# Kernel tuning notes

Measured on AMD Instinct MI355X. Metric: run time of the kernel, lower is better.

Reference implementation:

```python
import jax, jax.numpy as jnp
import numpy as np

WIN = 64
SHIFT = 32
HEADS = 12


def setup_inputs() -> dict:
    key = jax.random.key(0)
    ks = jax.random.split(key, 6)
    D = 768
    return {
        'x': jax.random.normal(ks[0], (16, 4096, D), dtype=jnp.float32),
        'qkv_w': jax.random.normal(ks[1], (3 * D, D), dtype=jnp.float32) * (D ** -0.5),
        'qkv_b': jax.random.normal(ks[2], (3 * D,), dtype=jnp.float32) * 0.02,
        'proj_w': jax.random.normal(ks[3], (D, D), dtype=jnp.float32) * (D ** -0.5),
        'proj_b': jax.random.normal(ks[4], (D,), dtype=jnp.float32) * 0.02,
        'rel_bias': jax.random.normal(ks[5], (HEADS, 2 * WIN - 1), dtype=jnp.float32) * 0.02,
    }


def reference(x, qkv_w, qkv_b, proj_w, proj_b, rel_bias):
    B, N, D = x.shape
    H, hd = HEADS, D // HEADS
    scale = hd ** -0.5
    if SHIFT:
        x = jnp.roll(x, SHIFT, axis=1)
    pad = (-N) % WIN
    if pad:
        x = jnp.pad(x, ((0, 0), (0, pad), (0, 0)))
    Np = x.shape[1]
    nW = Np // WIN
    # [B*nW, w, D] windows
    xw = x.reshape(B * nW, WIN, D)
    qkv = xw @ qkv_w.T + qkv_b                       # [B*nW, w, 3D]
    qkv = qkv.reshape(B * nW, WIN, 3, H, hd).transpose(2, 0, 3, 1, 4)
    q, k, v = qkv[0], qkv[1], qkv[2]                 # [B*nW, H, w, hd]
    attn = jnp.einsum('bhqd,bhkd->bhqk', q, k) * scale
    idx = jnp.arange(WIN)
    rel = idx[None, :] - idx[:, None] + (WIN - 1)    # [w, w] in [0, 2w-2]
    attn = attn + rel_bias[:, rel][None]             # gather bias per head
    attn = jax.nn.softmax(attn, axis=-1)
    y = jnp.einsum('bhqk,bhkd->bhqd', attn, v)       # [B*nW, H, w, hd]
    y = y.transpose(0, 2, 1, 3).reshape(B * nW, WIN, D)
    y = y @ proj_w.T + proj_b
    y = y.reshape(B, Np, D)
    if pad:
        y = y[:, :N, :]
    if SHIFT:
        y = jnp.roll(y, -SHIFT, axis=1)
    return y
```

## Files before the change

### kernel.cpp

```cpp
#include <hip/hip_runtime.h>
#include <hip/hip_bf16.h>
#include <stdint.h>

#define SEQ     4096
#define NBATCH  16
#define DMODEL  768
#define NHEAD   12
#define HDIM    64
#define WINSZ   64
#define SHIFT_T 32
#define QKV_N   (3*DMODEL)

typedef __attribute__((ext_vector_type(8)))  short bf16x8;
typedef __attribute__((ext_vector_type(4)))  float f32x4;

static __device__ __forceinline__ unsigned short f2bf(float f) {
  union { float f; unsigned u; } v; v.f = f;
  unsigned r = v.u + 0x7fffu + ((v.u >> 16) & 1u);
  return (unsigned short)(r >> 16);
}

#define G2L(gp, lp) __builtin_amdgcn_global_load_lds( \
    (const __attribute__((address_space(1))) unsigned*)(const void*)(gp), \
    (__attribute__((address_space(3))) unsigned*)(void*)(lp), 16, 0, 0)

#define MFMA16(a,b,c) __builtin_amdgcn_mfma_f32_16x16x32_bf16(a,b,c,0,0,0)
#define LDS8(p) (*(const bf16x8*)(p))
#define BARR __builtin_amdgcn_s_barrier()
#define SBAR __builtin_amdgcn_sched_barrier(0)
#define LGK0 do { asm volatile("s_waitcnt lgkmcnt(0)" ::: "memory"); SBAR; } while(0)

__global__ void k_cvt_x(const float* __restrict__ x, unsigned short* __restrict__ xb,
                        long long n8) {
  for (long long i = (long long)blockIdx.x*blockDim.x + threadIdx.x; i < n8;
       i += (long long)gridDim.x*blockDim.x) {
    long long e = i*8;
    int d = (int)(e % DMODEL);
    long long gt = e / DMODEL;
    int t = (int)(gt & (SEQ-1));
    long long b = gt >> 12;
    int ts = (t - SHIFT_T) & (SEQ-1);
    const float* src = x + (((b << 12) + ts) * (long long)DMODEL + d);
    float4 a0 = *(const float4*)src;
    float4 a1 = *(const float4*)(src + 4);
    bf16x8 o;
    o[0]=(short)f2bf(a0.x); o[1]=(short)f2bf(a0.y); o[2]=(short)f2bf(a0.z); o[3]=(short)f2bf(a0.w);
    o[4]=(short)f2bf(a1.x); o[5]=(short)f2bf(a1.y); o[6]=(short)f2bf(a1.z); o[7]=(short)f2bf(a1.w);
    *(bf16x8*)(xb + e) = o;
  }
}

__global__ void k_cvt_w(const float* __restrict__ w, unsigned short* __restrict__ wb, int n8) {
  int i = blockIdx.x*blockDim.x + threadIdx.x;
  if (i >= n8) return;
  float4 a0 = ((const float4*)w)[2*i];
  float4 a1 = ((const float4*)w)[2*i+1];
  bf16x8 o;
  o[0]=(short)f2bf(a0.x); o[1]=(short)f2bf(a0.y); o[2]=(short)f2bf(a0.z); o[3]=(short)f2bf(a0.w);
  o[4]=(short)f2bf(a1.x); o[5]=(short)f2bf(a1.y); o[6]=(short)f2bf(a1.z); o[7]=(short)f2bf(a1.w);
  ((bf16x8*)wb)[i] = o;
}

template<int MODE>
__global__ __launch_bounds__(512, 1)
void k_gemm256(const unsigned short* __restrict__ A, const unsigned short* __restrict__ Bw,
               const float* __restrict__ bias, unsigned short* __restrict__ Cb,
               float* __restrict__ Cf, int M, int N, int K, int nTN, long long c0) {
  __shared__ char lds[131072];
  const int nt = K >> 6;
  int nwg = gridDim.x;
  int cpx = nwg >> 3;
  int wg  = (blockIdx.x & 7) * cpx + (blockIdx.x >> 3);
  int bm = wg / nTN, bn = wg - bm*nTN;
  long long m0 = (long long)bm * 256;
  int n0 = bn * 256;
  int tid = threadIdx.x;
  int lane = tid & 63, wid = tid >> 6;
  int wr = wid >> 2, wc = wid & 3;
  int cl = lane & 15, g4 = lane >> 4;

  const long long K2 = 2LL * K;
  int L  = tid * 16;
  int Ls = L ^ (((L >> 7) & 7) << 4);
  int srow = Ls >> 7, scol = Ls & 127;
  const char* gAr0 = (const char*)A + (m0 +       srow) * K2 + scol;
  const char* gAr1 = (const char*)A + (m0 +  64 + srow) * K2 + scol;
  const char* gAr2 = (const char*)A + (m0 + 128 + srow) * K2 + scol;
  const char* gAr3 = (const char*)A + (m0 + 192 + srow) * K2 + scol;
  const char* gBr0 = (const char*)Bw + (long long)(n0 +       srow) * K2 + scol;
  const char* gBr1 = (const char*)Bw + (long long)(n0 +  64 + srow) * K2 + scol;
  const char* gBr2 = (const char*)Bw + (long long)(n0 + 128 + srow) * K2 + scol;
  const char* gBr3 = (const char*)Bw + (long long)(n0 + 192 + srow) * K2 + scol;

  int p0 = cl*128 + ((g4*16) ^ ((cl & 7) << 4));
  int p1 = p0 ^ 64;
  int RA0 = wr*16384;
  int RA1 = wr*16384 + 8192;
  int BB  = 32768 + wc*8192;

  f32x4 acc[8][4];
  #pragma unroll
  for (int i = 0; i < 8; ++i)
    #pragma unroll
    for (int j = 0; j < 4; ++j) acc[i][j] = (f32x4){0.f,0.f,0.f,0.f};

#define MMPH(MA, MB, x0, x1, y0, y1) \
  acc[MA][0]=MFMA16(x0,b00,acc[MA][0]); acc[MA][1]=MFMA16(x0,b10,acc[MA][1]); \
  acc[MA][2]=MFMA16(x0,b20,acc[MA][2]); acc[MA][3]=MFMA16(x0,b30,acc[MA][3]); \
  acc[MB][0]=MFMA16(y0,b00,acc[MB][0]); acc[MB][1]=MFMA16(y0,b10,acc[MB][1]); \
  acc[MB][2]=MFMA16(y0,b20,acc[MB][2]); acc[MB][3]=MFMA16(y0,b30,acc[MB][3]); \
  acc[MA][0]=MFMA16(x1,b01,acc[MA][0]); acc[MA][1]=MFMA16(x1,b11,acc[MA][1]); \
  acc[MA][2]=MFMA16(x1,b21,acc[MA][2]); acc[MA][3]=MFMA16(x1,b31,acc[MA][3]); \
  acc[MB][0]=MFMA16(y1,b01,acc[MB][0]); acc[MB][1]=MFMA16(y1,b11,acc[MB][1]); \
  acc[MB][2]=MFMA16(y1,b21,acc[MB][2]); acc[MB][3]=MFMA16(y1,b31,acc[MB][3]);

#define TILE(RD, ST, DOSTAGE, WBSTR, DOWA) do {                               \
    const char* rbuf = (RD); char* stb = (ST);                                \
    bf16x8 b00,b01,b10,b11,b20,b21,b30,b31;                                   \
    { bf16x8 x0 = LDS8(rbuf + RA0        + p0), x1 = LDS8(rbuf + RA0        + p1);\
      bf16x8 y0 = LDS8(rbuf + RA0 + 2048 + p0), y1 = LDS8(rbuf + RA0 + 2048 + p1);\
      b00 = LDS8(rbuf + BB        + p0);  b01 = LDS8(rbuf + BB        + p1);  \
      b10 = LDS8(rbuf + BB + 2048 + p0);  b11 = LDS8(rbuf + BB + 2048 + p1);  \
      b20 = LDS8(rbuf + BB + 4096 + p0);  b21 = LDS8(rbuf + BB + 4096 + p1);  \
      b30 = LDS8(rbuf + BB + 6144 + p0);  b31 = LDS8(rbuf + BB + 6144 + p1);  \
      if (DOSTAGE) { G2L(gBr0, stb + 32768 + L); G2L(gBr1, stb + 40960 + L); }\
      asm volatile("s_waitcnt lgkmcnt(8)" ::: "memory"); SBAR;                \
      BARR; LGK0;                                                             \
      __builtin_amdgcn_s_setprio(1);                                          \
      MMPH(0, 1, x0, x1, y0, y1)                                              \
      __builtin_amdgcn_s_setprio(0); SBAR; BARR;                              \
    }                                                                         \
    { bf16x8 x0 = LDS8(rbuf + RA0 + 4096 + p0), x1 = LDS8(rbuf + RA0 + 4096 + p1);\
      bf16x8 y0 = LDS8(rbuf + RA0 + 6144 + p0), y1 = LDS8(rbuf + RA0 + 6144 + p1);\
      if (DOSTAGE) { G2L(gBr2, stb + 49152 + L); G2L(gBr3, stb + 57344 + L); }\
      SBAR; BARR; LGK0;                                                       \
      __builtin_amdgcn_s_setprio(1);                                          \
      MMPH(2, 3, x0, x1, y0, y1)                                              \
      __builtin_amdgcn_s_setprio(0); SBAR;                                    \
      asm volatile(WBSTR ::: "memory"); SBAR; BARR;                           \
    }                                                                         \
    { bf16x8 x0 = LDS8(rbuf + RA1        + p0), x1 = LDS8(rbuf + RA1        + p1);\
      bf16x8 y0 = LDS8(rbuf + RA1 + 2048 + p0), y1 = LDS8(rbuf + RA1 + 2048 + p1);\
      if (DOSTAGE) { G2L(gAr0, stb + L); G2L(gAr2, stb + 16384 + L); }        \
      SBAR; BARR; LGK0;                                                       \
      __builtin_amdgcn_s_setprio(1);                                          \
      MMPH(4, 5, x0, x1, y0, y1)                                              \
      __builtin_amdgcn_s_setprio(0); SBAR; BARR;                              \
    }                                                                         \
    { bf16x8 x0 = LDS8(rbuf + RA1 + 4096 + p0), x1 = LDS8(rbuf + RA1 + 4096 + p1);\
      bf16x8 y0 = LDS8(rbuf + RA1 + 6144 + p0), y1 = LDS8(rbuf + RA1 + 6144 + p1);\
      if (DOSTAGE) { G2L(gAr1, stb + 8192 + L); G2L(gAr3, stb + 24576 + L);   \
                     gAr0 += 128; gAr1 += 128; gAr2 += 128; gAr3 += 128;      \
                     gBr0 += 128; gBr1 += 128; gBr2 += 128; gBr3 += 128; }    \
      SBAR; BARR; LGK0;                                                       \
      __builtin_amdgcn_s_setprio(1);                                          \
      MMPH(6, 7, x0, x1, y0, y1)                                              \
      __builtin_amdgcn_s_setprio(0); SBAR;                                    \
      if (DOWA) { asm volatile("s_waitcnt vmcnt(2)" ::: "memory"); }          \
      SBAR; BARR;                                                             \
    }                                                                         \
  } while (0)

  G2L(gBr0, lds + 32768 + L); G2L(gBr1, lds + 40960 + L);
  G2L(gBr2, lds + 49152 + L); G2L(gBr3, lds + 57344 + L);
  G2L(gAr0, lds + L);         G2L(gAr2, lds + 16384 + L);
  G2L(gAr1, lds + 8192 + L);  G2L(gAr3, lds + 24576 + L);
  gAr0 += 128; gAr1 += 128; gAr2 += 128; gAr3 += 128;
  gBr0 += 128; gBr1 += 128; gBr2 += 128; gBr3 += 128;
  asm volatile("s_waitcnt vmcnt(2)" ::: "memory");
  SBAR; BARR;

  char* const bufA = lds;
  char* const bufB = lds + 65536;
  for (int i = 0; i < (nt - 2) / 2; ++i) {
    TILE(bufA, bufB, 1, "s_waitcnt vmcnt(4)", 1);
    TILE(bufB, bufA, 1, "s_waitcnt vmcnt(4)", 1);
  }
  TILE(bufA, bufB, 1, "s_waitcnt vmcnt(4)", 1);
  TILE(bufB, bufA, 0, "s_waitcnt vmcnt(0)", 0);
#undef TILE
#undef MMPH

  #pragma unroll
  for (int mf = 0; mf < 8; ++mf) {
    #pragma unroll
    for (int nf = 0; nf < 4; ++nf) {
      int n = n0 + wc*64 + nf*16 + cl;
      float bv = bias[n];
      #pragma unroll
      for (int r = 0; r < 4; ++r) {
        long long m = m0 + wr*128 + mf*16 + g4*4 + r;
        float v = acc[mf][nf][r] + bv;
        if (MODE == 0) {
          int nb = n0 + wc*64;
          int t  = nb / DMODEL;
          int h  = (nb - t*DMODEL) >> 6;
          long long panel = ((((m >> 6)*NHEAD + h)*3 + t) << 12);
          Cb[panel + ((m & 63) << 6) + nf*16 + cl] = f2bf(v);
        } else {
          long long gm = c0 + m;
          long long om = (gm & ~(long long)(SEQ-1)) | ((gm - SHIFT_T) & (long long)(SEQ-1));
          Cf[om * (long long)N + n] = v;
        }
      }
    }
  }
}

__global__ __launch_bounds__(256, 4)
void k_attn(const unsigned short* __restrict__ qkv, const float* __restrict__ rel_bias,
            unsigned short* __restrict__ y) {
  int w = blockIdx.x / NHEAD;
  int h = blockIdx.x - w*NHEAD;
  __shared__ unsigned short sQ[64*72], sK[64*72], sV[64*72];
  __shared__ unsigned short sP[4][16*72];
  __shared__ float rb[128];
  int tid = threadIdx.x, lane = tid & 63, wid = tid >> 6;
  int cl = lane & 15, g4 = lane >> 4;

  if (tid < 2*WINSZ - 1) rb[tid] = rel_bias[h*(2*WINSZ-1) + tid];

  const unsigned short* panel = qkv + ((long long)((w*NHEAD + h)*3) << 12);
  {
    int row = tid >> 2, c16 = (tid & 3) * 16;
    const unsigned short* s0 = panel + tid*16;
    *(bf16x8*)(sQ + row*72 + c16)     = *(const bf16x8*)(s0);
    *(bf16x8*)(sQ + row*72 + c16 + 8) = *(const bf16x8*)(s0 + 8);
    *(bf16x8*)(sK + row*72 + c16)     = *(const bf16x8*)(s0 + 4096);
    *(bf16x8*)(sK + row*72 + c16 + 8) = *(const bf16x8*)(s0 + 4096 + 8);
    *(bf16x8*)(sV + row*72 + c16)     = *(const bf16x8*)(s0 + 8192);
    *(bf16x8*)(sV + row*72 + c16 + 8) = *(const bf16x8*)(s0 + 8192 + 8);
  }
  __syncthreads();

  f32x4 sc[4];
  #pragma unroll
  for (int nt = 0; nt < 4; ++nt) sc[nt] = (f32x4){0.f,0.f,0.f,0.f};
  #pragma unroll
  for (int kk = 0; kk < 2; ++kk) {
    bf16x8 aq = *(const bf16x8*)(sQ + (wid*16 + cl)*72 + kk*32 + g4*8);
    #pragma unroll
    for (int nt = 0; nt < 4; ++nt) {
      bf16x8 bk = *(const bf16x8*)(sK + (nt*16 + cl)*72 + kk*32 + g4*8);
      sc[nt] = MFMA16(aq, bk, sc[nt]);
    }
  }

  float pv[4][4];
  #pragma unroll
  for (int r = 0; r < 4; ++r) {
    int qi = wid*16 + g4*4 + r;
    float mx = -1e30f;
    #pragma unroll
    for (int nt = 0; nt < 4; ++nt) {
      int kj = nt*16 + cl;
      float v = sc[nt][r]*0.125f + rb[kj - qi + (WINSZ-1)];
      pv[nt][r] = v;
      mx = fmaxf(mx, v);
    }
    #pragma unroll
    for (int m = 1; m < 16; m <<= 1) mx = fmaxf(mx, __shfl_xor(mx, m, 64));
    float sum = 0.f;
    #pragma unroll
    for (int nt = 0; nt < 4; ++nt) { float e = __expf(pv[nt][r]-mx); pv[nt][r] = e; sum += e; }
    #pragma unroll
    for (int m = 1; m < 16; m <<= 1) sum += __shfl_xor(sum, m, 64);
    float inv = 1.f / sum;
    #pragma unroll
    for (int nt = 0; nt < 4; ++nt)
      sP[wid][(g4*4+r)*72 + nt*16 + cl] = f2bf(pv[nt][r]*inv);
  }

  f32x4 o[4];
  #pragma unroll
  for (int nt = 0; nt < 4; ++nt) o[nt] = (f32x4){0.f,0.f,0.f,0.f};
  #pragma unroll
  for (int kk = 0; kk < 2; ++kk) {
    bf16x8 ap = *(const bf16x8*)(&sP[wid][cl*72 + kk*32 + g4*8]);
    #pragma unroll
    for (int nt = 0; nt < 4; ++nt) {
      bf16x8 bv;
      #pragma unroll
      for (int j = 0; j < 8; ++j)
        bv[j] = (short)sV[(kk*32 + g4*8 + j)*72 + nt*16 + cl];
      o[nt] = MFMA16(ap, bv, o[nt]);
    }
  }

  long long tokbase = (long long)w * WINSZ;
  #pragma unroll
  for (int nt = 0; nt < 4; ++nt)
    #pragma unroll
    for (int r = 0; r < 4; ++r) {
      int row = wid*16 + g4*4 + r;
      y[(tokbase + row) * (long long)DMODEL + h*HDIM + nt*16 + cl] = f2bf(o[nt][r]);
    }
}

extern "C" void kernel_launch(void* const* d_in, const int* in_sizes, int n_in,
                              void* d_out, int out_size, void* d_ws, size_t ws_size,
                              hipStream_t stream) {
  const float* x      = (const float*)d_in[0];
  const float* qkv_w  = (const float*)d_in[1];
  const float* qkv_b  = (const float*)d_in[2];
  const float* proj_w = (const float*)d_in[3];
  const float* proj_b = (const float*)d_in[4];
  const float* rel_b  = (const float*)d_in[5];
  float* out = (float*)d_out;

  const long long NTOK = (long long)NBATCH * SEQ;

  char* ws = (char*)d_ws;
  unsigned short* qkvb = (unsigned short*)ws;
  unsigned short* yb   = (unsigned short*)(ws + (size_t)NTOK*QKV_N*2);
  unsigned short* wq   = (unsigned short*)(ws + (size_t)NTOK*QKV_N*2 + (size_t)NTOK*DMODEL*2);
  unsigned short* wp   = wq + (size_t)QKV_N*DMODEL;

  k_cvt_w<<<(QKV_N*DMODEL/8 + 255)/256, 256, 0, stream>>>(qkv_w, wq, QKV_N*DMODEL/8);
  k_cvt_w<<<(DMODEL*DMODEL/8 + 255)/256, 256, 0, stream>>>(proj_w, wp, DMODEL*DMODEL/8);

  long long n8 = NTOK * DMODEL / 8;
  k_cvt_x<<<2048, 256, 0, stream>>>(x, yb , n8);

  int mT = (int)(NTOK / 256);
  k_gemm256<0><<<mT * (QKV_N/256), 512, 0, stream>>>(yb, wq, qkv_b, qkvb, nullptr,
                                                     (int)NTOK, QKV_N, DMODEL, QKV_N/256, 0);
  k_attn<<<(int)(NTOK/WINSZ) * NHEAD, 256, 0, stream>>>(qkvb, rel_b, yb );
  k_gemm256<1><<<mT * (DMODEL/256), 512, 0, stream>>>(yb, wp, proj_b, nullptr, out,
                                                      (int)NTOK, DMODEL, DMODEL, DMODEL/256, 0);
}
```

Measured before the change: 498.6 us.

## Add dedicated 128x256 QKV GEMM kernel with triple-buffered LDS and higher occupancy

Replaces the 256x256 tile QKV projection GEMM with a new kernel using 128x256 tiles, a 3-stage LDS ring of 24KB per stage, and launch bounds allowing several workgroups per CU. The new kernel writes bf16 output directly in the per-window head-panel layout the attention kernel reads. The generic MODE 0 epilogue now writes row-major, but that path is no longer launched. The goal is better occupancy and latency hiding for the QKV GEMM. The cost is smaller tiles with less data reuse per workgroup and more workgroups.

```diff
diff --git a/kernel.cpp b/kernel.cpp
--- a/kernel.cpp
+++ b/kernel.cpp
@@ -59,6 +59,104 @@
   o[0]=(short)f2bf(a0.x); o[1]=(short)f2bf(a0.y); o[2]=(short)f2bf(a0.z); o[3]=(short)f2bf(a0.w);
   o[4]=(short)f2bf(a1.x); o[5]=(short)f2bf(a1.y); o[6]=(short)f2bf(a1.z); o[7]=(short)f2bf(a1.w);
   ((bf16x8*)wb)[i] = o;
+}
+
+__global__ __launch_bounds__(512, 4)
+void k_qkv128(const unsigned short* __restrict__ A, const unsigned short* __restrict__ Bw,
+              const float* __restrict__ bias, unsigned short* __restrict__ Cb) {
+  __shared__ char lds[3*24576];
+  const int nTN = QKV_N/256;
+  int nwg = gridDim.x;
+  int cpx = nwg >> 3;
+  int wg  = (blockIdx.x & 7) * cpx + (blockIdx.x >> 3);
+  int bm = wg / nTN, bn = wg - bm*nTN;
+  long long m0 = (long long)bm * 128;
+  int n0 = bn * 256;
+  int tid = threadIdx.x;
+  int lane = tid & 63, wid = tid >> 6;
+  int wr = wid >> 2, wc = wid & 3;
+  int cl = lane & 15, g4 = lane >> 4;
+
+  const long long K2 = 2LL * DMODEL;
+  int L  = tid * 16;
+  int Ls = L ^ (((L >> 7) & 7) << 4);
+  int srow = Ls >> 6, scol = Ls & 63;
+  const char* gA  = (const char*)A  + (m0 + srow) * K2 + scol;
+  const char* gB0 = (const char*)Bw + (long long)(n0 +       srow) * K2 + scol;
+  const char* gB1 = (const char*)Bw + (long long)(n0 + 128 + srow) * K2 + scol;
+
+  int key  = (cl >> 1) << 4;
+  int aoff = (wr*4096 + cl*64 + g4*16) ^ key;
+  int boff = 8192 + ((wc*4096 + cl*64 + g4*16) ^ key);
+
+  f32x4 acc[4][4];
+  #pragma unroll
+  for (int i = 0; i < 4; ++i)
+    #pragma unroll
+    for (int j = 0; j < 4; ++j) acc[i][j] = (f32x4){0.f,0.f,0.f,0.f};
+
+  G2L(gA,       lds + L);
+  G2L(gB0,      lds + 8192  + L);
+  G2L(gB1,      lds + 16384 + L);
+  G2L(gA  + 64, lds + 24576 + L);
+  G2L(gB0 + 64, lds + 24576 + 8192  + L);
+  G2L(gB1 + 64, lds + 24576 + 16384 + L);
+  gA += 128; gB0 += 128; gB1 += 128;
+  asm volatile("s_waitcnt vmcnt(3)" ::: "memory");
+  SBAR; BARR;
+
+#define QT(RS, SS, DOSTAGE, WSTR) do {                                        \
+    const char* rb = lds + (RS)*24576;                                        \
+    char* sb = lds + (SS)*24576;                                              \
+    if (DOSTAGE) { G2L(gA, sb + L); G2L(gB0, sb + 8192 + L);                  \
+                   G2L(gB1, sb + 16384 + L);                                  \
+                   gA += 64; gB0 += 64; gB1 += 64; }                          \
+    bf16x8 a0 = LDS8(rb + aoff);        bf16x8 a1 = LDS8(rb + aoff + 1024);   \
+    bf16x8 a2 = LDS8(rb + aoff + 2048); bf16x8 a3 = LDS8(rb + aoff + 3072);   \
+    bf16x8 b0 = LDS8(rb + boff);        bf16x8 b1 = LDS8(rb + boff + 1024);   \
+    bf16x8 b2 = LDS8(rb + boff + 2048); bf16x8 b3 = LDS8(rb + boff + 3072);   \
+    LGK0;                                                                     \
+    __builtin_amdgcn_s_setprio(1);                                            \
+    acc[0][0]=MFMA16(a0,b0,acc[0][0]); acc[0][1]=MFMA16(a0,b1,acc[0][1]);     \
+    acc[0][2]=MFMA16(a0,b2,acc[0][2]); acc[0][3]=MFMA16(a0,b3,acc[0][3]);     \
+    acc[1][0]=MFMA16(a1,b0,acc[1][0]); acc[1][1]=MFMA16(a1,b1,acc[1][1]);     \
+    acc[1][2]=MFMA16(a1,b2,acc[1][2]); acc[1][3]=MFMA16(a1,b3,acc[1][3]);     \
+    acc[2][0]=MFMA16(a2,b0,acc[2][0]); acc[2][1]=MFMA16(a2,b1,acc[2][1]);     \
+    acc[2][2]=MFMA16(a2,b2,acc[2][2]); acc[2][3]=MFMA16(a2,b3,acc[2][3]);     \
+    acc[3][0]=MFMA16(a3,b0,acc[3][0]); acc[3][1]=MFMA16(a3,b1,acc[3][1]);     \
+    acc[3][2]=MFMA16(a3,b2,acc[3][2]); acc[3][3]=MFMA16(a3,b3,acc[3][3]);     \
+    __builtin_amdgcn_s_setprio(0); SBAR;                                      \
+    asm volatile(WSTR ::: "memory"); SBAR;                                    \
+    BARR;                                                                     \
+  } while (0)
+
+  for (int i = 0; i < 7; ++i) {
+    QT(0, 2, 1, "s_waitcnt vmcnt(3)");
+    QT(1, 0, 1, "s_waitcnt vmcnt(3)");
+    QT(2, 1, 1, "s_waitcnt vmcnt(3)");
+  }
+  QT(0, 2, 1, "s_waitcnt vmcnt(3)");
+  QT(1, 0, 0, "s_waitcnt vmcnt(0)");
+  QT(2, 1, 0, "");
+#undef QT
+
+  #pragma unroll
+  for (int mf = 0; mf < 4; ++mf) {
+    #pragma unroll
+    for (int nf = 0; nf < 4; ++nf) {
+      int n = n0 + wc*64 + nf*16 + cl;
+      float bv = bias[n];
+      int nb = n0 + wc*64;
+      int t  = nb / DMODEL;
+      int h  = (nb - t*DMODEL) >> 6;
+      #pragma unroll
+      for (int r = 0; r < 4; ++r) {
+        long long m = m0 + wr*64 + mf*16 + g4*4 + r;
+        long long panel = ((((m >> 6)*NHEAD + h)*3 + t) << 12);
+        Cb[panel + ((m & 63) << 6) + nf*16 + cl] = f2bf(acc[mf][nf][r] + bv);
+      }
+    }
+  }
 }
 
 template<int MODE>
@@ -192,11 +290,7 @@
         long long m = m0 + wr*128 + mf*16 + g4*4 + r;
         float v = acc[mf][nf][r] + bv;
         if (MODE == 0) {
-          int nb = n0 + wc*64;
-          int t  = nb / DMODEL;
-          int h  = (nb - t*DMODEL) >> 6;
-          long long panel = ((((m >> 6)*NHEAD + h)*3 + t) << 12);
-          Cb[panel + ((m & 63) << 6) + nf*16 + cl] = f2bf(v);
+          Cb[m * (long long)N + n] = f2bf(v);
         } else {
           long long gm = c0 + m;
           long long om = (gm & ~(long long)(SEQ-1)) | ((gm - SHIFT_T) & (long long)(SEQ-1));
@@ -322,10 +416,11 @@
   long long n8 = NTOK * DMODEL / 8;
   k_cvt_x<<<2048, 256, 0, stream>>>(x, yb , n8);
 
+  k_qkv128<<<4608, 512, 0, stream>>>(yb, wq, qkv_b, qkvb);
+
+  k_attn<<<(int)(NTOK/WINSZ) * NHEAD, 256, 0, stream>>>(qkvb, rel_b, yb );
+
   int mT = (int)(NTOK / 256);
-  k_gemm256<0><<<mT * (QKV_N/256), 512, 0, stream>>>(yb, wq, qkv_b, qkvb, nullptr,
-                                                     (int)NTOK, QKV_N, DMODEL, QKV_N/256, 0);
-  k_attn<<<(int)(NTOK/WINSZ) * NHEAD, 256, 0, stream>>>(qkvb, rel_b, yb );
   k_gemm256<1><<<mT * (DMODEL/256), 512, 0, stream>>>(yb, wp, proj_b, nullptr, out,
                                                       (int)NTOK, DMODEL, DMODEL, DMODEL/256, 0);
 }
```

Measured after the change: 517.0 us. 3.7% more time.
